# Kernel optimization log

Measured on AMD Instinct MI355X. Metric: run time of the kernel, lower is better.

## Reference

```python
import jax, jax.numpy as jnp
import numpy as np

B, H, S, D = 4, 16, 4096, 64

def _phi(x):
    # feature map for linear attention: elu(x) + 1 (positive features)
    return jax.nn.elu(x) + 1.0

def setup_inputs() -> dict:
    key = jax.random.key(0)
    kq, kk, kv = jax.random.split(key, 3)
    return {
        "query": jax.random.normal(kq, (B, H, S, D), dtype=jnp.float32),
        "key": jax.random.normal(kk, (B, H, S, D), dtype=jnp.float32),
        "value": jax.random.normal(kv, (B, H, S, D), dtype=jnp.float32),
        "attention_mask": jnp.ones((B, S), dtype=jnp.float32),
    }

def reference(query, key, value, attention_mask):
    head_dim = query.shape[-1]
    scale = 1.0 / jnp.sqrt(jnp.sqrt(jnp.float32(head_dim)))
    q = query * scale
    k = key * scale
    phi_q = _phi(q)
    phi_k = _phi(k)
    m = attention_mask[:, None, :, None]  # [B,1,S,1]
    phi_q = phi_q * m
    phi_k = phi_k * m
    # kv_term: [B,H,D,Dv]
    kv_term = jnp.einsum("bhsd,bhse->bhde", phi_k, value)
    out = jnp.einsum("bhsd,bhde->bhse", phi_q, kv_term)
    # normalizer: phi_q @ sum_s phi_k -> [B,H,S,1]
    k_one = jnp.sum(phi_k, axis=-2)  # [B,H,D]
    normalizer = jnp.einsum("bhsd,bhd->bhs", phi_q, k_one)[..., None]
    return out / (normalizer + 1e-8)
```

## Files before the change

### kernel.cpp

```cpp
#include <hip/hip_runtime.h>

#define BDIM 4
#define HDIM 16
#define SDIM 4096
#define DDIM 64
#define NBH (BDIM * HDIM)

#define P1_TS 16
#define BH_STRIDE (DDIM * DDIM + DDIM)
#define CHUNK_FLOATS (NBH * BH_STRIDE)
#define P2_MT 128

__device__ __forceinline__ float phi_f(float x) {
    return x > 0.0f ? x + 1.0f : __expf(x);
}

template<bool ATOMIC>
__global__ __launch_bounds__(256) void la_phase1(
    const float* __restrict__ K, const float* __restrict__ V,
    const float* __restrict__ mask, float* __restrict__ outp, int chunk_rows)
{
    __shared__ float kT[2][P1_TS][DDIM];
    __shared__ float vT[2][P1_TS][DDIM];

    const int bh  = blockIdx.y;
    const int b   = bh / HDIM;
    const int t   = threadIdx.x;
    const int row = t >> 4;
    const int c4  = (t & 15) << 2;
    const int d0  = row << 2;
    const int e0  = c4;
    const int s_base = blockIdx.x * chunk_rows;

    const float* Kb = K + (size_t)bh * SDIM * DDIM;
    const float* Vb = V + (size_t)bh * SDIM * DDIM;
    const float* mb = mask + (size_t)b * SDIM;

    const float scale = 0.35355339059327373f;

    float acc[4][4] = {};
    float k1[4] = {0.f, 0.f, 0.f, 0.f};

    int s0 = s_base + row;
    float4 kf = *(const float4*)(Kb + (size_t)s0 * DDIM + c4);
    float4 vf = *(const float4*)(Vb + (size_t)s0 * DDIM + c4);
    float  m  = mb[s0];

    const int ntiles = chunk_rows >> 4;
    int p = 0;
    for (int tt = 0; tt < ntiles; ++tt) {
        const float p0 = phi_f(kf.x * scale) * m;
        const float p1 = phi_f(kf.y * scale) * m;
        const float p2 = phi_f(kf.z * scale) * m;
        const float p3 = phi_f(kf.w * scale) * m;
        kT[p][row][c4 + 0] = p0;
        kT[p][row][c4 + 1] = p1;
        kT[p][row][c4 + 2] = p2;
        kT[p][row][c4 + 3] = p3;
        *(float4*)&vT[p][row][c4] = vf;
        k1[0] += p0; k1[1] += p1; k1[2] += p2; k1[3] += p3;
        __syncthreads();

        if (tt + 1 < ntiles) {
            const int sn = s_base + ((tt + 1) << 4) + row;
            kf = *(const float4*)(Kb + (size_t)sn * DDIM + c4);
            vf = *(const float4*)(Vb + (size_t)sn * DDIM + c4);
            m  = mb[sn];
        }

        #pragma unroll
        for (int ss = 0; ss < P1_TS; ++ss) {
            const float4 a  = *(const float4*)&kT[p][ss][d0];
            const float4 v4 = *(const float4*)&vT[p][ss][e0];
            acc[0][0] += a.x * v4.x; acc[0][1] += a.x * v4.y; acc[0][2] += a.x * v4.z; acc[0][3] += a.x * v4.w;
            acc[1][0] += a.y * v4.x; acc[1][1] += a.y * v4.y; acc[1][2] += a.y * v4.z; acc[1][3] += a.y * v4.w;
            acc[2][0] += a.z * v4.x; acc[2][1] += a.z * v4.y; acc[2][2] += a.z * v4.z; acc[2][3] += a.z * v4.w;
            acc[3][0] += a.w * v4.x; acc[3][1] += a.w * v4.y; acc[3][2] += a.w * v4.z; acc[3][3] += a.w * v4.w;
        }
        p ^= 1;
    }

    float* base = ATOMIC ? (outp + (size_t)bh * BH_STRIDE)
                         : (outp + ((size_t)blockIdx.x * NBH + bh) * BH_STRIDE);
    if (ATOMIC) {
        #pragma unroll
        for (int i = 0; i < 4; ++i)
            #pragma unroll
            for (int j = 0; j < 4; ++j)
                atomicAdd(&base[(d0 + i) * DDIM + e0 + j], acc[i][j]);
    } else {
        #pragma unroll
        for (int i = 0; i < 4; ++i)
            *(float4*)&base[(d0 + i) * DDIM + e0] =
                make_float4(acc[i][0], acc[i][1], acc[i][2], acc[i][3]);
    }

    __syncthreads();
    kT[0][row][c4 + 0] = k1[0];
    kT[0][row][c4 + 1] = k1[1];
    kT[0][row][c4 + 2] = k1[2];
    kT[0][row][c4 + 3] = k1[3];
    __syncthreads();
    if (t < DDIM) {
        float s1 = 0.f;
        #pragma unroll
        for (int r = 0; r < P1_TS; ++r) s1 += kT[0][r][t];
        if (ATOMIC) atomicAdd(&base[DDIM * DDIM + t], s1);
        else        base[DDIM * DDIM + t] = s1;
    }
}

__global__ __launch_bounds__(256) void la_reduce(
    const float* __restrict__ part, float* __restrict__ fin, int nc)
{
    const int g = blockIdx.x * 256 + threadIdx.x;
    const float4* p4 = (const float4*)part;
    float4 s = p4[g];
    for (int c = 1; c < nc; ++c) {
        const float4 v = p4[(size_t)c * (CHUNK_FLOATS / 4) + g];
        s.x += v.x; s.y += v.y; s.z += v.z; s.w += v.w;
    }
    ((float4*)fin)[g] = s;
}

__global__ __launch_bounds__(512) void la_phase2(
    const float* __restrict__ Q, const float* __restrict__ mask,
    const float* __restrict__ fin_all, float* __restrict__ out)
{
    __shared__ float kvL[DDIM][DDIM];
    __shared__ float pqT[DDIM][P2_MT + 4];
    __shared__ float koL[DDIM];

    const int bh = blockIdx.y;
    const int b  = bh / HDIM;
    const int t  = threadIdx.x;
    const int s_base = blockIdx.x * P2_MT;

    const float scale = 0.35355339059327373f;
    const float* fin = fin_all + (size_t)bh * BH_STRIDE;

    {
        const float4* src = (const float4*)fin;
        float4* dst = (float4*)&kvL[0][0];
        dst[t] = src[t];
        dst[t + 512] = src[t + 512];
        if (t < DDIM) koL[t] = fin[DDIM * DDIM + t];
    }
    {
        const float* Qb = Q + (size_t)bh * SDIM * DDIM;
        const float* mb = mask + (size_t)b * SDIM;
        const int lr   = t & 15;
        const int c4   = ((t >> 4) & 15) << 2;
        const int half = t >> 8;
        #pragma unroll
        for (int k = 0; k < 4; ++k) {
            const int r = lr + 16 * (half * 4 + k);
            const int s = s_base + r;
            const float4 qf = *(const float4*)(Qb + (size_t)s * DDIM + c4);
            const float mm = mb[s];
            pqT[c4 + 0][r] = phi_f(qf.x * scale) * mm;
            pqT[c4 + 1][r] = phi_f(qf.y * scale) * mm;
            pqT[c4 + 2][r] = phi_f(qf.z * scale) * mm;
            pqT[c4 + 3][r] = phi_f(qf.w * scale) * mm;
        }
    }
    __syncthreads();

    const int r0 = (t >> 4) << 2;
    const int e0 = (t & 15) << 2;
    float acc[4][4] = {};
    float nrm[4] = {0.f, 0.f, 0.f, 0.f};

    #pragma unroll 16
    for (int d = 0; d < DDIM; ++d) {
        const float4 a  = *(const float4*)&pqT[d][r0];
        const float4 bb = *(const float4*)&kvL[d][e0];
        const float ko = koL[d];
        acc[0][0] += a.x * bb.x; acc[0][1] += a.x * bb.y; acc[0][2] += a.x * bb.z; acc[0][3] += a.x * bb.w;
        acc[1][0] += a.y * bb.x; acc[1][1] += a.y * bb.y; acc[1][2] += a.y * bb.z; acc[1][3] += a.y * bb.w;
        acc[2][0] += a.z * bb.x; acc[2][1] += a.z * bb.y; acc[2][2] += a.z * bb.z; acc[2][3] += a.z * bb.w;
        acc[3][0] += a.w * bb.x; acc[3][1] += a.w * bb.y; acc[3][2] += a.w * bb.z; acc[3][3] += a.w * bb.w;
        nrm[0] += a.x * ko; nrm[1] += a.y * ko; nrm[2] += a.z * ko; nrm[3] += a.w * ko;
    }

    float* ob = out + ((size_t)bh * SDIM + s_base) * DDIM;
    #pragma unroll
    for (int i = 0; i < 4; ++i) {
        const float inv = 1.0f / (nrm[i] + 1e-8f);
        float4 o;
        o.x = acc[i][0] * inv;
        o.y = acc[i][1] * inv;
        o.z = acc[i][2] * inv;
        o.w = acc[i][3] * inv;
        *(float4*)(ob + (size_t)(r0 + i) * DDIM + e0) = o;
    }
}

extern "C" void kernel_launch(void* const* d_in, const int* in_sizes, int n_in,
                              void* d_out, int out_size, void* d_ws, size_t ws_size,
                              hipStream_t stream) {
    const float* Q = (const float*)d_in[0];
    const float* K = (const float*)d_in[1];
    const float* V = (const float*)d_in[2];
    const float* M = (const float*)d_in[3];
    float* out = (float*)d_out;

    const size_t chunk_bytes = (size_t)CHUNK_FLOATS * sizeof(float);

    int nc = 0;
    if      (ws_size >= 33 * chunk_bytes) nc = 32;
    else if (ws_size >= 17 * chunk_bytes) nc = 16;

    if (nc > 0) {
        float* part = (float*)d_ws;
        float* fin  = part + (size_t)nc * CHUNK_FLOATS;
        la_phase1<false><<<dim3(nc, NBH), dim3(256), 0, stream>>>(K, V, M, part, SDIM / nc);
        la_reduce<<<dim3(CHUNK_FLOATS / 4 / 256), dim3(256), 0, stream>>>(part, fin, nc);
        la_phase2<<<dim3(SDIM / P2_MT, NBH), dim3(512), 0, stream>>>(Q, M, fin, out);
    } else {
        float* fin = (float*)d_ws;
        hipMemsetAsync(d_ws, 0, chunk_bytes, stream);
        la_phase1<true><<<dim3(16, NBH), dim3(256), 0, stream>>>(K, V, M, fin, SDIM / 16);
        la_phase2<<<dim3(SDIM / P2_MT, NBH), dim3(512), 0, stream>>>(Q, M, fin, out);
    }
}
```

Before: 249.1 us.

## Rewrite linear attention kernels with per-wave 8x8 register tiles and direct global loads

```diff
diff --git a/kernel.cpp b/kernel.cpp
--- a/kernel.cpp
+++ b/kernel.cpp
@@ -6,193 +6,231 @@
 #define DDIM 64
 #define NBH (BDIM * HDIM)
 
-#define P1_TS 16
+#define NC 16
 #define BH_STRIDE (DDIM * DDIM + DDIM)
 #define CHUNK_FLOATS (NBH * BH_STRIDE)
-#define P2_MT 128
 
 __device__ __forceinline__ float phi_f(float x) {
     return x > 0.0f ? x + 1.0f : __expf(x);
 }
 
 template<bool ATOMIC>
-__global__ __launch_bounds__(256) void la_phase1(
+__global__ __launch_bounds__(256, 4) void la_phase1(
     const float* __restrict__ K, const float* __restrict__ V,
     const float* __restrict__ mask, float* __restrict__ outp, int chunk_rows)
 {
-    __shared__ float kT[2][P1_TS][DDIM];
-    __shared__ float vT[2][P1_TS][DDIM];
-
-    const int bh  = blockIdx.y;
-    const int b   = bh / HDIM;
-    const int t   = threadIdx.x;
-    const int row = t >> 4;
-    const int c4  = (t & 15) << 2;
-    const int d0  = row << 2;
-    const int e0  = c4;
-    const int s_base = blockIdx.x * chunk_rows;
+    __shared__ __align__(16) float smem[8320];
+
+    const int bh = blockIdx.y;
+    const int b  = bh / HDIM;
+    const int t  = threadIdx.x;
+    const int w  = t >> 6;
+    const int l  = t & 63;
+    const int rowq = l >> 4;
+    const int c4   = (l & 15) << 2;
+    const int d0   = (l >> 3) << 3;
+    const int e0   = (l & 7) << 3;
+
+    float* kT = smem + w * 2080;
 
     const float* Kb = K + (size_t)bh * SDIM * DDIM;
     const float* Vb = V + (size_t)bh * SDIM * DDIM;
     const float* mb = mask + (size_t)b * SDIM;
-
     const float scale = 0.35355339059327373f;
 
-    float acc[4][4] = {};
-    float k1[4] = {0.f, 0.f, 0.f, 0.f};
-
-    int s0 = s_base + row;
-    float4 kf = *(const float4*)(Kb + (size_t)s0 * DDIM + c4);
-    float4 vf = *(const float4*)(Vb + (size_t)s0 * DDIM + c4);
-    float  m  = mb[s0];
-
-    const int ntiles = chunk_rows >> 4;
-    int p = 0;
+    const int rows_per_wave = chunk_rows >> 2;
+    const int s_wave = blockIdx.x * chunk_rows + w * rows_per_wave;
+    const int ntiles = rows_per_wave >> 4;
+
+    float acc[8][8] = {};
+    float k1s[4] = {0.f, 0.f, 0.f, 0.f};
+
+    float4 kr[4]; float mmr[4];
+    #pragma unroll
+    for (int j = 0; j < 4; ++j) {
+        const int s = s_wave + rowq + (j << 2);
+        kr[j]  = *(const float4*)(Kb + (size_t)s * DDIM + c4);
+        mmr[j] = mb[s];
+    }
+
     for (int tt = 0; tt < ntiles; ++tt) {
-        const float p0 = phi_f(kf.x * scale) * m;
-        const float p1 = phi_f(kf.y * scale) * m;
-        const float p2 = phi_f(kf.z * scale) * m;
-        const float p3 = phi_f(kf.w * scale) * m;
-        kT[p][row][c4 + 0] = p0;
-        kT[p][row][c4 + 1] = p1;
-        kT[p][row][c4 + 2] = p2;
-        kT[p][row][c4 + 3] = p3;
-        *(float4*)&vT[p][row][c4] = vf;
-        k1[0] += p0; k1[1] += p1; k1[2] += p2; k1[3] += p3;
-        __syncthreads();
-
+        #pragma unroll
+        for (int j = 0; j < 4; ++j) {
+            float4 p;
+            p.x = phi_f(kr[j].x * scale) * mmr[j];
+            p.y = phi_f(kr[j].y * scale) * mmr[j];
+            p.z = phi_f(kr[j].z * scale) * mmr[j];
+            p.w = phi_f(kr[j].w * scale) * mmr[j];
+            k1s[0] += p.x; k1s[1] += p.y; k1s[2] += p.z; k1s[3] += p.w;
+            *(float4*)&kT[(rowq + (j << 2)) * DDIM + c4] = p;
+        }
         if (tt + 1 < ntiles) {
-            const int sn = s_base + ((tt + 1) << 4) + row;
-            kf = *(const float4*)(Kb + (size_t)sn * DDIM + c4);
-            vf = *(const float4*)(Vb + (size_t)sn * DDIM + c4);
-            m  = mb[sn];
-        }
-
-        #pragma unroll
-        for (int ss = 0; ss < P1_TS; ++ss) {
-            const float4 a  = *(const float4*)&kT[p][ss][d0];
-            const float4 v4 = *(const float4*)&vT[p][ss][e0];
-            acc[0][0] += a.x * v4.x; acc[0][1] += a.x * v4.y; acc[0][2] += a.x * v4.z; acc[0][3] += a.x * v4.w;
-            acc[1][0] += a.y * v4.x; acc[1][1] += a.y * v4.y; acc[1][2] += a.y * v4.z; acc[1][3] += a.y * v4.w;
-            acc[2][0] += a.z * v4.x; acc[2][1] += a.z * v4.y; acc[2][2] += a.z * v4.z; acc[2][3] += a.z * v4.w;
-            acc[3][0] += a.w * v4.x; acc[3][1] += a.w * v4.y; acc[3][2] += a.w * v4.z; acc[3][3] += a.w * v4.w;
-        }
-        p ^= 1;
-    }
+            #pragma unroll
+            for (int j = 0; j < 4; ++j) {
+                const int s = s_wave + ((tt + 1) << 4) + rowq + (j << 2);
+                kr[j]  = *(const float4*)(Kb + (size_t)s * DDIM + c4);
+                mmr[j] = mb[s];
+            }
+        }
+        asm volatile("s_waitcnt lgkmcnt(0)" ::: "memory");
+
+        const int s_tile = s_wave + (tt << 4);
+        #pragma unroll
+        for (int ss = 0; ss < 16; ++ss) {
+            const float4 a0 = *(const float4*)&kT[ss * DDIM + d0];
+            const float4 a1 = *(const float4*)&kT[ss * DDIM + d0 + 4];
+            const float4 v0 = *(const float4*)(Vb + (size_t)(s_tile + ss) * DDIM + e0);
+            const float4 v1 = *(const float4*)(Vb + (size_t)(s_tile + ss) * DDIM + e0 + 4);
+            const float av[8] = {a0.x, a0.y, a0.z, a0.w, a1.x, a1.y, a1.z, a1.w};
+            const float vv[8] = {v0.x, v0.y, v0.z, v0.w, v1.x, v1.y, v1.z, v1.w};
+            #pragma unroll
+            for (int i = 0; i < 8; ++i)
+                #pragma unroll
+                for (int j = 0; j < 8; ++j)
+                    acc[i][j] += av[i] * vv[j];
+        }
+        asm volatile("" ::: "memory");
+    }
+
+    #pragma unroll
+    for (int i = 0; i < 4; ++i) {
+        k1s[i] += __shfl_xor(k1s[i], 16);
+        k1s[i] += __shfl_xor(k1s[i], 32);
+    }
+
+    __syncthreads();
+    float* bufA = smem;
+    float* bufB = smem + 4160;
+    if (w < 2) {
+        float* Bp = w ? bufB : bufA;
+        #pragma unroll
+        for (int i = 0; i < 8; ++i) {
+            *(float4*)&Bp[(d0 + i) * DDIM + e0]     = make_float4(acc[i][0], acc[i][1], acc[i][2], acc[i][3]);
+            *(float4*)&Bp[(d0 + i) * DDIM + e0 + 4] = make_float4(acc[i][4], acc[i][5], acc[i][6], acc[i][7]);
+        }
+        if (l < 16) *(float4*)&Bp[4096 + (l << 2)] = make_float4(k1s[0], k1s[1], k1s[2], k1s[3]);
+    }
+    __syncthreads();
+    if (w >= 2) {
+        float* Bp = (w == 3) ? bufB : bufA;
+        #pragma unroll
+        for (int i = 0; i < 8; ++i) {
+            float4 x0 = *(float4*)&Bp[(d0 + i) * DDIM + e0];
+            float4 x1 = *(float4*)&Bp[(d0 + i) * DDIM + e0 + 4];
+            x0.x += acc[i][0]; x0.y += acc[i][1]; x0.z += acc[i][2]; x0.w += acc[i][3];
+            x1.x += acc[i][4]; x1.y += acc[i][5]; x1.z += acc[i][6]; x1.w += acc[i][7];
+            *(float4*)&Bp[(d0 + i) * DDIM + e0]     = x0;
+            *(float4*)&Bp[(d0 + i) * DDIM + e0 + 4] = x1;
+        }
+        if (l < 16) {
+            float4 x = *(float4*)&Bp[4096 + (l << 2)];
+            x.x += k1s[0]; x.y += k1s[1]; x.z += k1s[2]; x.w += k1s[3];
+            *(float4*)&Bp[4096 + (l << 2)] = x;
+        }
+    }
+    __syncthreads();
 
     float* base = ATOMIC ? (outp + (size_t)bh * BH_STRIDE)
                          : (outp + ((size_t)blockIdx.x * NBH + bh) * BH_STRIDE);
-    if (ATOMIC) {
-        #pragma unroll
-        for (int i = 0; i < 4; ++i)
-            #pragma unroll
-            for (int j = 0; j < 4; ++j)
-                atomicAdd(&base[(d0 + i) * DDIM + e0 + j], acc[i][j]);
-    } else {
-        #pragma unroll
-        for (int i = 0; i < 4; ++i)
-            *(float4*)&base[(d0 + i) * DDIM + e0] =
-                make_float4(acc[i][0], acc[i][1], acc[i][2], acc[i][3]);
-    }
-
-    __syncthreads();
-    kT[0][row][c4 + 0] = k1[0];
-    kT[0][row][c4 + 1] = k1[1];
-    kT[0][row][c4 + 2] = k1[2];
-    kT[0][row][c4 + 3] = k1[3];
-    __syncthreads();
-    if (t < DDIM) {
-        float s1 = 0.f;
-        #pragma unroll
-        for (int r = 0; r < P1_TS; ++r) s1 += kT[0][r][t];
-        if (ATOMIC) atomicAdd(&base[DDIM * DDIM + t], s1);
-        else        base[DDIM * DDIM + t] = s1;
+    for (int g = t; g < BH_STRIDE / 4; g += 256) {
+        const float4 xa = ((const float4*)bufA)[g];
+        const float4 xb = ((const float4*)bufB)[g];
+        if (ATOMIC) {
+            atomicAdd(&base[4 * g + 0], xa.x + xb.x);
+            atomicAdd(&base[4 * g + 1], xa.y + xb.y);
+            atomicAdd(&base[4 * g + 2], xa.z + xb.z);
+            atomicAdd(&base[4 * g + 3], xa.w + xb.w);
+        } else {
+            *(float4*)&base[4 * g] = make_float4(xa.x + xb.x, xa.y + xb.y, xa.z + xb.z, xa.w + xb.w);
+        }
     }
 }
 
 __global__ __launch_bounds__(256) void la_reduce(
-    const float* __restrict__ part, float* __restrict__ fin, int nc)
+    const float* __restrict__ part, float* __restrict__ fin)
 {
     const int g = blockIdx.x * 256 + threadIdx.x;
     const float4* p4 = (const float4*)part;
     float4 s = p4[g];
-    for (int c = 1; c < nc; ++c) {
+    #pragma unroll
+    for (int c = 1; c < NC; ++c) {
         const float4 v = p4[(size_t)c * (CHUNK_FLOATS / 4) + g];
         s.x += v.x; s.y += v.y; s.z += v.z; s.w += v.w;
     }
     ((float4*)fin)[g] = s;
 }
 
-__global__ __launch_bounds__(512) void la_phase2(
+__global__ __launch_bounds__(256, 4) void la_phase2(
     const float* __restrict__ Q, const float* __restrict__ mask,
     const float* __restrict__ fin_all, float* __restrict__ out)
 {
-    __shared__ float kvL[DDIM][DDIM];
-    __shared__ float pqT[DDIM][P2_MT + 4];
-    __shared__ float koL[DDIM];
+    __shared__ __align__(16) float kvL[DDIM * DDIM];
+    __shared__ __align__(16) float koL[DDIM];
 
     const int bh = blockIdx.y;
     const int b  = bh / HDIM;
     const int t  = threadIdx.x;
-    const int s_base = blockIdx.x * P2_MT;
-
-    const float scale = 0.35355339059327373f;
+    const int w  = t >> 6;
+    const int l  = t & 63;
+    const int e0 = (l & 7) << 3;
+    const int r0 = blockIdx.x * 256 + (w << 6) + ((l >> 3) << 3);
+
     const float* fin = fin_all + (size_t)bh * BH_STRIDE;
-
     {
         const float4* src = (const float4*)fin;
-        float4* dst = (float4*)&kvL[0][0];
-        dst[t] = src[t];
-        dst[t + 512] = src[t + 512];
+        float4* dst = (float4*)kvL;
+        #pragma unroll
+        for (int k = 0; k < 4; ++k) dst[t + 256 * k] = src[t + 256 * k];
         if (t < DDIM) koL[t] = fin[DDIM * DDIM + t];
     }
-    {
-        const float* Qb = Q + (size_t)bh * SDIM * DDIM;
-        const float* mb = mask + (size_t)b * SDIM;
-        const int lr   = t & 15;
-        const int c4   = ((t >> 4) & 15) << 2;
-        const int half = t >> 8;
-        #pragma unroll
-        for (int k = 0; k < 4; ++k) {
-            const int r = lr + 16 * (half * 4 + k);
-            const int s = s_base + r;
-            const float4 qf = *(const float4*)(Qb + (size_t)s * DDIM + c4);
-            const float mm = mb[s];
-            pqT[c4 + 0][r] = phi_f(qf.x * scale) * mm;
-            pqT[c4 + 1][r] = phi_f(qf.y * scale) * mm;
-            pqT[c4 + 2][r] = phi_f(qf.z * scale) * mm;
-            pqT[c4 + 3][r] = phi_f(qf.w * scale) * mm;
-        }
-    }
-    __syncthreads();
-
-    const int r0 = (t >> 4) << 2;
-    const int e0 = (t & 15) << 2;
-    float acc[4][4] = {};
-    float nrm[4] = {0.f, 0.f, 0.f, 0.f};
-
-    #pragma unroll 16
-    for (int d = 0; d < DDIM; ++d) {
-        const float4 a  = *(const float4*)&pqT[d][r0];
-        const float4 bb = *(const float4*)&kvL[d][e0];
-        const float ko = koL[d];
-        acc[0][0] += a.x * bb.x; acc[0][1] += a.x * bb.y; acc[0][2] += a.x * bb.z; acc[0][3] += a.x * bb.w;
-        acc[1][0] += a.y * bb.x; acc[1][1] += a.y * bb.y; acc[1][2] += a.y * bb.z; acc[1][3] += a.y * bb.w;
-        acc[2][0] += a.z * bb.x; acc[2][1] += a.z * bb.y; acc[2][2] += a.z * bb.z; acc[2][3] += a.z * bb.w;
-        acc[3][0] += a.w * bb.x; acc[3][1] += a.w * bb.y; acc[3][2] += a.w * bb.z; acc[3][3] += a.w * bb.w;
-        nrm[0] += a.x * ko; nrm[1] += a.y * ko; nrm[2] += a.z * ko; nrm[3] += a.w * ko;
-    }
-
-    float* ob = out + ((size_t)bh * SDIM + s_base) * DDIM;
-    #pragma unroll
-    for (int i = 0; i < 4; ++i) {
-        const float inv = 1.0f / (nrm[i] + 1e-8f);
-        float4 o;
-        o.x = acc[i][0] * inv;
-        o.y = acc[i][1] * inv;
-        o.z = acc[i][2] * inv;
-        o.w = acc[i][3] * inv;
-        *(float4*)(ob + (size_t)(r0 + i) * DDIM + e0) = o;
+    __syncthreads();
+
+    const float* Qb = Q + (size_t)bh * SDIM * DDIM;
+    const float* mb = mask + (size_t)b * SDIM;
+    const float scale = 0.35355339059327373f;
+
+    float acc[8][8] = {};
+    float nrm[8] = {0.f, 0.f, 0.f, 0.f, 0.f, 0.f, 0.f, 0.f};
+
+    #pragma unroll 1
+    for (int dt = 0; dt < 16; ++dt) {
+        const int d4 = dt << 2;
+        float4 qp[8];
+        #pragma unroll
+        for (int i = 0; i < 8; ++i) {
+            const float4 q = *(const float4*)(Qb + (size_t)(r0 + i) * DDIM + d4);
+            qp[i].x = phi_f(q.x * scale);
+            qp[i].y = phi_f(q.y * scale);
+            qp[i].z = phi_f(q.z * scale);
+            qp[i].w = phi_f(q.w * scale);
+        }
+        const float4 ko4 = *(const float4*)&koL[d4];
+        #pragma unroll
+        for (int dd = 0; dd < 4; ++dd) {
+            const float4 b0 = *(const float4*)&kvL[(d4 + dd) * DDIM + e0];
+            const float4 b1 = *(const float4*)&kvL[(d4 + dd) * DDIM + e0 + 4];
+            const float bv[8] = {b0.x, b0.y, b0.z, b0.w, b1.x, b1.y, b1.z, b1.w};
+            const float kod = (dd == 0) ? ko4.x : (dd == 1) ? ko4.y : (dd == 2) ? ko4.z : ko4.w;
+            #pragma unroll
+            for (int i = 0; i < 8; ++i) {
+                const float a = (dd == 0) ? qp[i].x : (dd == 1) ? qp[i].y : (dd == 2) ? qp[i].z : qp[i].w;
+                nrm[i] += a * kod;
+                #pragma unroll
+                for (int j = 0; j < 8; ++j)
+                    acc[i][j] += a * bv[j];
+            }
+        }
+    }
+
+    float* ob = out + (size_t)bh * SDIM * DDIM;
+    #pragma unroll
+    for (int i = 0; i < 8; ++i) {
+        const float mm  = mb[r0 + i];
+        const float inv = mm / (mm * nrm[i] + 1e-8f);
+        *(float4*)(ob + (size_t)(r0 + i) * DDIM + e0) =
+            make_float4(acc[i][0] * inv, acc[i][1] * inv, acc[i][2] * inv, acc[i][3] * inv);
+        *(float4*)(ob + (size_t)(r0 + i) * DDIM + e0 + 4) =
+            make_float4(acc[i][4] * inv, acc[i][5] * inv, acc[i][6] * inv, acc[i][7] * inv);
     }
 }
 
@@ -207,20 +245,16 @@
 
     const size_t chunk_bytes = (size_t)CHUNK_FLOATS * sizeof(float);
 
-    int nc = 0;
-    if      (ws_size >= 33 * chunk_bytes) nc = 32;
-    else if (ws_size >= 17 * chunk_bytes) nc = 16;
-
-    if (nc > 0) {
+    if (ws_size >= (size_t)(NC + 1) * chunk_bytes) {
         float* part = (float*)d_ws;
-        float* fin  = part + (size_t)nc * CHUNK_FLOATS;
-        la_phase1<false><<<dim3(nc, NBH), dim3(256), 0, stream>>>(K, V, M, part, SDIM / nc);
-        la_reduce<<<dim3(CHUNK_FLOATS / 4 / 256), dim3(256), 0, stream>>>(part, fin, nc);
-        la_phase2<<<dim3(SDIM / P2_MT, NBH), dim3(512), 0, stream>>>(Q, M, fin, out);
+        float* fin  = part + (size_t)NC * CHUNK_FLOATS;
+        la_phase1<false><<<dim3(NC, NBH), dim3(256), 0, stream>>>(K, V, M, part, SDIM / NC);
+        la_reduce<<<dim3(CHUNK_FLOATS / 4 / 256), dim3(256), 0, stream>>>(part, fin);
+        la_phase2<<<dim3(SDIM / 256, NBH), dim3(256), 0, stream>>>(Q, M, fin, out);
     } else {
         float* fin = (float*)d_ws;
         hipMemsetAsync(d_ws, 0, chunk_bytes, stream);
-        la_phase1<true><<<dim3(16, NBH), dim3(256), 0, stream>>>(K, V, M, fin, SDIM / 16);
-        la_phase2<<<dim3(SDIM / P2_MT, NBH), dim3(512), 0, stream>>>(Q, M, fin, out);
-    }
-}
+        la_phase1<true><<<dim3(NC, NBH), dim3(256), 0, stream>>>(K, V, M, fin, SDIM / NC);
+        la_phase2<<<dim3(SDIM / 256, NBH), dim3(256), 0, stream>>>(Q, M, fin, out);
+    }
+}
```

After: 450.4 us. 1.81x slower.
